# Optimization experiments

Measured on AMD Instinct MI355X. Metric: run time of the kernel, lower is better.

## Reference

```python
import jax, jax.numpy as jnp
import numpy as np

K = 1  # top-k experts per image


def cv_squared(v):
    # squared coefficient of variation; torch .var() is unbiased -> ddof=1
    eps = 1e-10
    m = v.mean()
    var = v.var(ddof=1)
    return jnp.where(jnp.abs(m) < eps, jnp.zeros((), v.dtype), var / (m * m + eps))


def setup_inputs() -> dict:
    key = jax.random.key(0)
    k0, k1, k2, k3 = jax.random.split(key, 4)
    B, H, W, C, E, HID = 64, 32, 32, 512, 5, 2048
    x = jax.random.normal(k0, (B, H, W, C), jnp.float32)
    # xavier-uniform-like scale for the gate
    gate_scale = float(np.sqrt(6.0 / (C + E)))
    w_gate = jax.random.uniform(k1, (C, E), jnp.float32, -gate_scale, gate_scale)
    W1 = jax.random.normal(k2, (E, C, HID), jnp.float32) * 0.02
    b1 = jnp.zeros((E, HID), jnp.float32)
    W2 = jax.random.normal(k3, (E, HID, C), jnp.float32) * 0.02
    b2 = jnp.zeros((E, C), jnp.float32)
    return {"x": x, "w_gate": w_gate, "W1": W1, "b1": b1, "W2": W2, "b2": b2}


def reference(x, w_gate, W1, b1, W2, b2):
    B, H, W_, C = x.shape
    E = w_gate.shape[1]
    xt = x.reshape(B, H * W_, C)              # [B, T, C] tokens
    xg = x.mean(axis=(1, 2))                  # [B, C] per-image gating feature

    # eval-mode noisy_top_k_gating (no noise): clean logits, clamp, top-k softmax
    logits = jnp.clip(xg @ w_gate, -50.0, 50.0)          # [B, E]
    top_logits, top_idx = jax.lax.top_k(logits, min(K + 1, E))
    tk_logits = top_logits[:, :K]
    tk_idx = top_idx[:, :K]                               # [B, K]
    tk_gates = jax.nn.softmax(tk_logits, axis=1)          # [B, K]
    gates = jnp.zeros_like(logits).at[jnp.arange(B)[:, None], tk_idx].set(tk_gates)

    importance = gates.sum(axis=0)                        # [E]
    load = (gates > 0).sum(axis=0).astype(jnp.float32)    # [E]
    loss = jnp.clip(cv_squared(importance) + cv_squared(load), 0.0, 1000.0)

    # dispatch: every token of image b goes through its top-K experts
    y = jnp.zeros_like(xt)
    for ki in range(K):
        idx = tk_idx[:, ki]                               # [B] expert id per image
        h = jnp.einsum('btd,bdh->bth', xt, W1[idx]) + b1[idx][:, None, :]
        h = jax.nn.gelu(h, approximate=False)             # torch nn.GELU default (erf)
        o = jnp.einsum('bth,bhd->btd', h, W2[idx]) + b2[idx][:, None, :]
        y = y + tk_gates[:, ki][:, None, None] * o

    return y.reshape(B, H, W_, C), loss
```

## Files before the change

### kernel.cpp

```cpp
#include <hip/hip_runtime.h>
#include <hip/hip_bf16.h>
#include <math.h>

typedef __attribute__((ext_vector_type(4))) float f4_t;
typedef __attribute__((ext_vector_type(8))) short s8_t;

constexpr int Bc = 64;
constexpr int Tc = 1024;
constexpr int Cc = 512;
constexpr int Ec = 5;
constexpr int HIDc = 2048;

__device__ __forceinline__ void async_copy16(const void* gsrc, void* ldst) {
  __builtin_amdgcn_global_load_lds(
      (const __attribute__((address_space(1))) unsigned int*)gsrc,
      (__attribute__((address_space(3))) unsigned int*)ldst, 16, 0, 0);
}


__global__ void k_partial(const float* __restrict__ x, float* __restrict__ part) {
  int b = blockIdx.x, p = blockIdx.y, tid = threadIdx.x;
  const float* xp = x + ((size_t)b * Tc + (size_t)p * 128) * Cc;
  float s0 = 0.f, s1 = 0.f;
  for (int t = 0; t < 128; ++t) {
    s0 += xp[(size_t)t * Cc + tid];
    s1 += xp[(size_t)t * Cc + tid + 256];
  }
  part[(size_t)(b * 8 + p) * Cc + tid] = s0;
  part[(size_t)(b * 8 + p) * Cc + tid + 256] = s1;
}

__global__ void k_xg_logits(const float* __restrict__ part, const float* __restrict__ wg,
                            float* __restrict__ logits) {
  __shared__ float xg[Cc];
  __shared__ float red[Ec][4];
  int b = blockIdx.x, tid = threadIdx.x;
  for (int c = tid; c < Cc; c += 256) {
    float s = 0.f;
#pragma unroll
    for (int p = 0; p < 8; ++p) s += part[(size_t)(b * 8 + p) * Cc + c];
    xg[c] = s * (1.0f / 1024.0f);
  }
  __syncthreads();
  float le[Ec] = {0.f, 0.f, 0.f, 0.f, 0.f};
  for (int c = tid; c < Cc; c += 256) {
    float v = xg[c];
#pragma unroll
    for (int e = 0; e < Ec; ++e) le[e] += v * wg[c * Ec + e];
  }
#pragma unroll
  for (int e = 0; e < Ec; ++e) {
    float v = le[e];
#pragma unroll
    for (int off = 32; off > 0; off >>= 1) v += __shfl_down(v, off);
    if ((tid & 63) == 0) red[e][tid >> 6] = v;
  }
  __syncthreads();
  if (tid < Ec) {
    float v = red[tid][0] + red[tid][1] + red[tid][2] + red[tid][3];
    v = fminf(fmaxf(v, -50.f), 50.f);
    logits[b * Ec + tid] = v;
  }
}

__global__ void k_gate(const float* __restrict__ logits, int* __restrict__ idx,
                       float* __restrict__ loss_out) {
  __shared__ int cnt[Ec];
  int tid = threadIdx.x;
  if (tid < Ec) cnt[tid] = 0;
  __syncthreads();
  if (tid < Bc) {
    const float* lb = logits + tid * Ec;
    int best = 0;
    float bv = lb[0];
#pragma unroll
    for (int e = 1; e < Ec; ++e) {
      float v = lb[e];
      if (v > bv) { bv = v; best = e; }
    }
    idx[tid] = best;
    atomicAdd(&cnt[best], 1);
  }
  __syncthreads();
  if (tid == 0) {
    const float mean = (float)Bc / (float)Ec;
    float var = 0.f;
#pragma unroll
    for (int e = 0; e < Ec; ++e) {
      float d = (float)cnt[e] - mean;
      var += d * d;
    }
    var *= (1.0f / (Ec - 1));
    float loss = 2.f * (var / (mean * mean + 1e-10f));
    loss = fminf(fmaxf(loss, 0.f), 1000.f);
    *loss_out = loss;
  }
}

__global__ void k_transpose_cvt(const float* __restrict__ src, __hip_bfloat16* __restrict__ dst,
                                int K, int N) {
  __shared__ float tile[32][33];
  int e = blockIdx.z;
  int kb = blockIdx.y * 32, nb = blockIdx.x * 32;
  const float* s = src + (size_t)e * K * N;
  __hip_bfloat16* d = dst + (size_t)e * K * N;
  int lx = threadIdx.x & 31, ly = threadIdx.x >> 5;
#pragma unroll
  for (int r = 0; r < 4; ++r) {
    int k = kb + ly + r * 8;
    tile[ly + r * 8][lx] = s[(size_t)k * N + nb + lx];
  }
  __syncthreads();
#pragma unroll
  for (int r = 0; r < 4; ++r) {
    int n = nb + ly + r * 8;
    d[(size_t)n * K + kb + lx] = __float2bfloat16(tile[lx][ly + r * 8]);
  }
}

__global__ void k_cvt_x(const float* __restrict__ src, ushort* __restrict__ dst, int n4) {
  int i = blockIdx.x * blockDim.x + threadIdx.x;
  int stride = gridDim.x * blockDim.x;
  const float4* s4 = (const float4*)src;
  ushort4* d4 = (ushort4*)dst;
  for (; i < n4; i += stride) {
    float4 v = s4[i];
    union { __hip_bfloat16 h[4]; ushort4 u; } cv;
    cv.h[0] = __float2bfloat16(v.x);
    cv.h[1] = __float2bfloat16(v.y);
    cv.h[2] = __float2bfloat16(v.z);
    cv.h[3] = __float2bfloat16(v.w);
    d4[i] = cv.u;
  }
}


__global__ __launch_bounds__(512, 2) void k_gemm1(
    const __hip_bfloat16* __restrict__ xbf, const __hip_bfloat16* __restrict__ w1t,
    const float* __restrict__ b1, const int* __restrict__ idx, int b0,
    __hip_bfloat16* __restrict__ h) {
  constexpr int K = Cc;
  constexpr int N = HIDc;
  constexpr int NT = K / 64;
  __shared__ short lds[2][2][256 * 64];

  int bz = blockIdx.z;
  int e = idx[b0 + bz];
  int m0 = blockIdx.y * 256;
  int n0 = blockIdx.x * 256;
  const short* Abase = (const short*)xbf + ((size_t)bz * Tc + m0) * K;
  const short* Bbase = (const short*)w1t + ((size_t)e * N + n0) * K;
  int tid = threadIdx.x;
  int l = tid & 63, w = tid >> 6;
  int wr = w >> 2, wc = w & 3;

  int s_row = tid >> 3;
  int s_col = (tid & 7) * 8;
  const short* gA[4];
  const short* gB[4];
#pragma unroll
  for (int i = 0; i < 4; ++i) {
    gA[i] = Abase + (size_t)(i * 64 + s_row) * K + s_col;
    gB[i] = Bbase + (size_t)(i * 64 + s_row) * K + s_col;
  }

  int a_off = (wr * 128 + (l & 15)) * 64 + (l >> 4) * 8;
  int b_off = (wc * 64 + (l & 15)) * 64 + (l >> 4) * 8;

  f4_t acc[8][4] = {};

#pragma unroll
  for (int i = 0; i < 4; ++i) {
    async_copy16(gA[i], (char*)&lds[0][0][0] + tid * 16 + i * 8192);
    async_copy16(gB[i], (char*)&lds[0][1][0] + tid * 16 + i * 8192);
  }
  __syncthreads();

  for (int t = 0; t < NT; ++t) {
    int cur = t & 1;
    const short* As = &lds[cur][0][0];
    const short* Bs = &lds[cur][1][0];
    if (t + 1 < NT) {
      int k0 = (t + 1) * 64;
#pragma unroll
      for (int i = 0; i < 4; ++i) {
        async_copy16(gA[i] + k0, (char*)&lds[cur ^ 1][0][0] + tid * 16 + i * 8192);
        async_copy16(gB[i] + k0, (char*)&lds[cur ^ 1][1][0] + tid * 16 + i * 8192);
      }
    }
#pragma unroll
    for (int kk = 0; kk < 2; ++kk) {
      s8_t a[8], b[4];
#pragma unroll
      for (int f = 0; f < 8; ++f)
        a[f] = *(const s8_t*)(As + a_off + f * 16 * 64 + kk * 32);
#pragma unroll
      for (int f = 0; f < 4; ++f)
        b[f] = *(const s8_t*)(Bs + b_off + f * 16 * 64 + kk * 32);
#pragma unroll
      for (int fm = 0; fm < 8; ++fm)
#pragma unroll
        for (int fn = 0; fn < 4; ++fn)
          acc[fm][fn] = __builtin_amdgcn_mfma_f32_16x16x32_bf16(a[fm], b[fn], acc[fm][fn], 0, 0, 0);
    }
    if (t + 1 < NT) __syncthreads();
  }

  __syncthreads();
  __hip_bfloat16* chunk = (__hip_bfloat16*)&lds[0][0][0] + w * 8192;
  const float* bias = b1 + (size_t)e * N;
#pragma unroll
  for (int fn = 0; fn < 4; ++fn) {
    int col = n0 + wc * 64 + fn * 16 + (l & 15);
    float bv = bias[col];
#pragma unroll
    for (int fm = 0; fm < 8; ++fm) {
      int row = fm * 16 + ((l >> 4) << 2);
#pragma unroll
      for (int j = 0; j < 4; ++j) {
        float v = acc[fm][fn][j] + bv;
        v = 0.5f * v * (1.0f + erff(v * 0.70710678118654752f));
        chunk[(row + j) * 64 + fn * 16 + (l & 15)] = __float2bfloat16(v);
      }
    }
  }
  short* hb = (short*)(h + (size_t)bz * Tc * N);
  int colb = n0 + wc * 64 + (l & 7) * 8;
#pragma unroll
  for (int p = 0; p < 16; ++p) {
    int row = p * 8 + (l >> 3);
    s8_t vrow = *(const s8_t*)((const short*)chunk + row * 64 + (l & 7) * 8);
    *(s8_t*)(hb + (size_t)(m0 + wr * 128 + row) * N + colb) = vrow;
  }
}

__global__ __launch_bounds__(512, 2) void k_gemm2(
    const __hip_bfloat16* __restrict__ h, const __hip_bfloat16* __restrict__ w2t,
    const float* __restrict__ b2, const int* __restrict__ idx, int b0,
    float* __restrict__ out) {
  constexpr int K = HIDc;
  constexpr int N = Cc;
  constexpr int NT = K / 64;
  __shared__ short lds[2][2][256 * 64];

  int bz = blockIdx.z;
  int e = idx[b0 + bz];
  int m0 = blockIdx.y * 256;
  int n0 = blockIdx.x * 256;
  const short* Abase = (const short*)h + ((size_t)bz * Tc + m0) * K;
  const short* Bbase = (const short*)w2t + ((size_t)e * N + n0) * K;
  int tid = threadIdx.x;
  int l = tid & 63, w = tid >> 6;
  int wr = w >> 2, wc = w & 3;

  int s_row = tid >> 3;
  int s_col = (tid & 7) * 8;
  const short* gA[4];
  const short* gB[4];
#pragma unroll
  for (int i = 0; i < 4; ++i) {
    gA[i] = Abase + (size_t)(i * 64 + s_row) * K + s_col;
    gB[i] = Bbase + (size_t)(i * 64 + s_row) * K + s_col;
  }

  int a_off = (wr * 128 + (l & 15)) * 64 + (l >> 4) * 8;
  int b_off = (wc * 64 + (l & 15)) * 64 + (l >> 4) * 8;

  f4_t acc[8][4] = {};

#pragma unroll
  for (int i = 0; i < 4; ++i) {
    async_copy16(gA[i], (char*)&lds[0][0][0] + tid * 16 + i * 8192);
    async_copy16(gB[i], (char*)&lds[0][1][0] + tid * 16 + i * 8192);
  }
  __syncthreads();

  for (int t = 0; t < NT; ++t) {
    int cur = t & 1;
    const short* As = &lds[cur][0][0];
    const short* Bs = &lds[cur][1][0];
    if (t + 1 < NT) {
      int k0 = (t + 1) * 64;
#pragma unroll
      for (int i = 0; i < 4; ++i) {
        async_copy16(gA[i] + k0, (char*)&lds[cur ^ 1][0][0] + tid * 16 + i * 8192);
        async_copy16(gB[i] + k0, (char*)&lds[cur ^ 1][1][0] + tid * 16 + i * 8192);
      }
    }
#pragma unroll
    for (int kk = 0; kk < 2; ++kk) {
      s8_t a[8], b[4];
#pragma unroll
      for (int f = 0; f < 8; ++f)
        a[f] = *(const s8_t*)(As + a_off + f * 16 * 64 + kk * 32);
#pragma unroll
      for (int f = 0; f < 4; ++f)
        b[f] = *(const s8_t*)(Bs + b_off + f * 16 * 64 + kk * 32);
#pragma unroll
      for (int fm = 0; fm < 8; ++fm)
#pragma unroll
        for (int fn = 0; fn < 4; ++fn)
          acc[fm][fn] = __builtin_amdgcn_mfma_f32_16x16x32_bf16(a[fm], b[fn], acc[fm][fn], 0, 0, 0);
    }
    if (t + 1 < NT) __syncthreads();
  }

  float* ob = out + (size_t)(b0 + bz) * Tc * N;
  const float* bias = b2 + (size_t)e * N;
#pragma unroll
  for (int fn = 0; fn < 4; ++fn) {
    int col = n0 + wc * 64 + fn * 16 + (l & 15);
    float bv = bias[col];
#pragma unroll
    for (int fm = 0; fm < 8; ++fm) {
      int rbase = m0 + wr * 128 + fm * 16 + ((l >> 4) << 2);
#pragma unroll
      for (int j = 0; j < 4; ++j) {
        ob[(size_t)(rbase + j) * N + col] = acc[fm][fn][j] + bv;
      }
    }
  }
}

extern "C" void kernel_launch(void* const* d_in, const int* in_sizes, int n_in,
                              void* d_out, int out_size, void* d_ws, size_t ws_size,
                              hipStream_t stream) {
  const float* x  = (const float*)d_in[0];
  const float* wg = (const float*)d_in[1];
  const float* W1 = (const float*)d_in[2];
  const float* b1 = (const float*)d_in[3];
  const float* W2 = (const float*)d_in[4];
  const float* b2 = (const float*)d_in[5];
  float* out = (float*)d_out;

  char* ws = (char*)d_ws;
  size_t off = 0;
  float* part = (float*)(ws + off); off += (size_t)Bc * 8 * Cc * 4;
  float* logits = (float*)(ws + off); off += (size_t)Bc * Ec * 4;
  int* idx = (int*)(ws + off); off += (size_t)Bc * 4;
  off = (off + 255) & ~(size_t)255;
  __hip_bfloat16* w1t = (__hip_bfloat16*)(ws + off); off += (size_t)Ec * HIDc * Cc * 2;
  __hip_bfloat16* w2t = (__hip_bfloat16*)(ws + off); off += (size_t)Ec * HIDc * Cc * 2;
  size_t dynoff = (off + 255) & ~(size_t)255;

  const size_t x_per_b = (size_t)Tc * Cc * 2;
  const size_t h_per_b = (size_t)Tc * HIDc * 2;
  size_t avail = ws_size > dynoff ? ws_size - dynoff : 0;
  int cb = (int)(avail / (x_per_b + h_per_b));
  if (cb > Bc) cb = Bc;
  if (cb < 1) cb = 1;

  k_partial<<<dim3(Bc, 8), 256, 0, stream>>>(x, part);
  k_xg_logits<<<dim3(Bc), 256, 0, stream>>>(part, wg, logits);
  k_gate<<<dim3(1), 256, 0, stream>>>(logits, idx, out + ((size_t)out_size - 1));

  k_transpose_cvt<<<dim3(HIDc / 32, Cc / 32, Ec), 256, 0, stream>>>(W1, w1t, Cc, HIDc);
  k_transpose_cvt<<<dim3(Cc / 32, HIDc / 32, Ec), 256, 0, stream>>>(W2, w2t, HIDc, Cc);

  __hip_bfloat16* xbf = (__hip_bfloat16*)(ws + dynoff);
  __hip_bfloat16* hbf = (__hip_bfloat16*)(ws + dynoff + (size_t)cb * x_per_b);

  for (int b0 = 0; b0 < Bc; b0 += cb) {
    int c = (Bc - b0) < cb ? (Bc - b0) : cb;
    int n4 = c * (Tc * Cc / 4);
    k_cvt_x<<<dim3(1024), 256, 0, stream>>>(x + (size_t)b0 * Tc * Cc, (ushort*)xbf, n4);
    k_gemm1<<<dim3(HIDc / 256, Tc / 256, c), 512, 0, stream>>>(xbf, w1t, b1, idx, b0, hbf);
    k_gemm2<<<dim3(Cc / 256, Tc / 256, c), 512, 0, stream>>>(hbf, w2t, b2, idx, b0, out);
  }
}
```

Before: 527.3 us.

## Fuse x mean and bf16 conversion, swizzle LDS, retile gemm1, cheaper GELU

After: 495.1 us. -6.1%, faster.

```diff
diff --git a/kernel.cpp b/kernel.cpp
--- a/kernel.cpp
+++ b/kernel.cpp
@@ -17,6 +17,47 @@
       (__attribute__((address_space(3))) unsigned int*)ldst, 16, 0, 0);
 }
 
+__device__ __forceinline__ float gelu_f(float v) {
+  float u = v * 0.70710678118654752f;
+  float ax = fabsf(u);
+  float t = __frcp_rn(1.0f + 0.3275911f * ax);
+  float p = t * (0.254829592f +
+           t * (-0.284496736f +
+           t * (1.421413741f +
+           t * (-1.453152027f +
+           t * 1.061405429f))));
+  float er = 1.0f - p * __expf(-u * u);
+  er = copysignf(er, u);
+  return 0.5f * v * (1.0f + er);
+}
+
+
+__global__ void k_prep(const float* __restrict__ x, ushort* __restrict__ xbf,
+                       float* __restrict__ part) {
+  int b = blockIdx.x, p = blockIdx.y, tid = threadIdx.x;
+  const float4* xp = (const float4*)(x + ((size_t)b * Tc + (size_t)p * 128) * Cc);
+  ushort4* op = (ushort4*)(xbf + ((size_t)b * Tc + (size_t)p * 128) * Cc);
+  int c4 = tid & 127, r0 = tid >> 7;
+  float4 s = {0.f, 0.f, 0.f, 0.f};
+  for (int r = r0; r < 128; r += 2) {
+    float4 v = xp[(size_t)r * 128 + c4];
+    s.x += v.x; s.y += v.y; s.z += v.z; s.w += v.w;
+    union { __hip_bfloat16 h[4]; ushort4 u; } cv;
+    cv.h[0] = __float2bfloat16(v.x);
+    cv.h[1] = __float2bfloat16(v.y);
+    cv.h[2] = __float2bfloat16(v.z);
+    cv.h[3] = __float2bfloat16(v.w);
+    op[(size_t)r * 128 + c4] = cv.u;
+  }
+  __shared__ float4 sh[128];
+  if (r0) sh[c4] = s;
+  __syncthreads();
+  if (!r0) {
+    float4 o = sh[c4];
+    s.x += o.x; s.y += o.y; s.z += o.z; s.w += o.w;
+    ((float4*)part)[(size_t)(b * 8 + p) * 128 + c4] = s;
+  }
+}
 
 __global__ void k_partial(const float* __restrict__ x, float* __restrict__ part) {
   int b = blockIdx.x, p = blockIdx.y, tid = threadIdx.x;
@@ -28,94 +69,6 @@
   }
   part[(size_t)(b * 8 + p) * Cc + tid] = s0;
   part[(size_t)(b * 8 + p) * Cc + tid + 256] = s1;
-}
-
-__global__ void k_xg_logits(const float* __restrict__ part, const float* __restrict__ wg,
-                            float* __restrict__ logits) {
-  __shared__ float xg[Cc];
-  __shared__ float red[Ec][4];
-  int b = blockIdx.x, tid = threadIdx.x;
-  for (int c = tid; c < Cc; c += 256) {
-    float s = 0.f;
-#pragma unroll
-    for (int p = 0; p < 8; ++p) s += part[(size_t)(b * 8 + p) * Cc + c];
-    xg[c] = s * (1.0f / 1024.0f);
-  }
-  __syncthreads();
-  float le[Ec] = {0.f, 0.f, 0.f, 0.f, 0.f};
-  for (int c = tid; c < Cc; c += 256) {
-    float v = xg[c];
-#pragma unroll
-    for (int e = 0; e < Ec; ++e) le[e] += v * wg[c * Ec + e];
-  }
-#pragma unroll
-  for (int e = 0; e < Ec; ++e) {
-    float v = le[e];
-#pragma unroll
-    for (int off = 32; off > 0; off >>= 1) v += __shfl_down(v, off);
-    if ((tid & 63) == 0) red[e][tid >> 6] = v;
-  }
-  __syncthreads();
-  if (tid < Ec) {
-    float v = red[tid][0] + red[tid][1] + red[tid][2] + red[tid][3];
-    v = fminf(fmaxf(v, -50.f), 50.f);
-    logits[b * Ec + tid] = v;
-  }
-}
-
-__global__ void k_gate(const float* __restrict__ logits, int* __restrict__ idx,
-                       float* __restrict__ loss_out) {
-  __shared__ int cnt[Ec];
-  int tid = threadIdx.x;
-  if (tid < Ec) cnt[tid] = 0;
-  __syncthreads();
-  if (tid < Bc) {
-    const float* lb = logits + tid * Ec;
-    int best = 0;
-    float bv = lb[0];
-#pragma unroll
-    for (int e = 1; e < Ec; ++e) {
-      float v = lb[e];
-      if (v > bv) { bv = v; best = e; }
-    }
-    idx[tid] = best;
-    atomicAdd(&cnt[best], 1);
-  }
-  __syncthreads();
-  if (tid == 0) {
-    const float mean = (float)Bc / (float)Ec;
-    float var = 0.f;
-#pragma unroll
-    for (int e = 0; e < Ec; ++e) {
-      float d = (float)cnt[e] - mean;
-      var += d * d;
-    }
-    var *= (1.0f / (Ec - 1));
-    float loss = 2.f * (var / (mean * mean + 1e-10f));
-    loss = fminf(fmaxf(loss, 0.f), 1000.f);
-    *loss_out = loss;
-  }
-}
-
-__global__ void k_transpose_cvt(const float* __restrict__ src, __hip_bfloat16* __restrict__ dst,
-                                int K, int N) {
-  __shared__ float tile[32][33];
-  int e = blockIdx.z;
-  int kb = blockIdx.y * 32, nb = blockIdx.x * 32;
-  const float* s = src + (size_t)e * K * N;
-  __hip_bfloat16* d = dst + (size_t)e * K * N;
-  int lx = threadIdx.x & 31, ly = threadIdx.x >> 5;
-#pragma unroll
-  for (int r = 0; r < 4; ++r) {
-    int k = kb + ly + r * 8;
-    tile[ly + r * 8][lx] = s[(size_t)k * N + nb + lx];
-  }
-  __syncthreads();
-#pragma unroll
-  for (int r = 0; r < 4; ++r) {
-    int n = nb + ly + r * 8;
-    d[(size_t)n * K + kb + lx] = __float2bfloat16(tile[lx][ly + r * 8]);
-  }
 }
 
 __global__ void k_cvt_x(const float* __restrict__ src, ushort* __restrict__ dst, int n4) {
@@ -134,175 +87,275 @@
   }
 }
 
-
-__global__ __launch_bounds__(512, 2) void k_gemm1(
+__global__ void k_xg_logits(const float* __restrict__ part, const float* __restrict__ wg,
+                            float* __restrict__ logits) {
+  __shared__ float xg[Cc];
+  __shared__ float red[Ec][4];
+  int b = blockIdx.x, tid = threadIdx.x;
+  for (int c = tid; c < Cc; c += 256) {
+    float s = 0.f;
+#pragma unroll
+    for (int p = 0; p < 8; ++p) s += part[(size_t)(b * 8 + p) * Cc + c];
+    xg[c] = s * (1.0f / 1024.0f);
+  }
+  __syncthreads();
+  float le[Ec] = {0.f, 0.f, 0.f, 0.f, 0.f};
+  for (int c = tid; c < Cc; c += 256) {
+    float v = xg[c];
+#pragma unroll
+    for (int e = 0; e < Ec; ++e) le[e] += v * wg[c * Ec + e];
+  }
+#pragma unroll
+  for (int e = 0; e < Ec; ++e) {
+    float v = le[e];
+#pragma unroll
+    for (int off = 32; off > 0; off >>= 1) v += __shfl_down(v, off);
+    if ((tid & 63) == 0) red[e][tid >> 6] = v;
+  }
+  __syncthreads();
+  if (tid < Ec) {
+    float v = red[tid][0] + red[tid][1] + red[tid][2] + red[tid][3];
+    v = fminf(fmaxf(v, -50.f), 50.f);
+    logits[b * Ec + tid] = v;
+  }
+}
+
+__global__ void k_gate(const float* __restrict__ logits, int* __restrict__ idx,
+                       float* __restrict__ loss_out) {
+  __shared__ int cnt[Ec];
+  int tid = threadIdx.x;
+  if (tid < Ec) cnt[tid] = 0;
+  __syncthreads();
+  if (tid < Bc) {
+    const float* lb = logits + tid * Ec;
+    int best = 0;
+    float bv = lb[0];
+#pragma unroll
+    for (int e = 1; e < Ec; ++e) {
+      float v = lb[e];
+      if (v > bv) { bv = v; best = e; }
+    }
+    idx[tid] = best;
+    atomicAdd(&cnt[best], 1);
+  }
+  __syncthreads();
+  if (tid == 0) {
+    const float mean = (float)Bc / (float)Ec;
+    float var = 0.f;
+#pragma unroll
+    for (int e = 0; e < Ec; ++e) {
+      float d = (float)cnt[e] - mean;
+      var += d * d;
+    }
+    var *= (1.0f / (Ec - 1));
+    float loss = 2.f * (var / (mean * mean + 1e-10f));
+    loss = fminf(fmaxf(loss, 0.f), 1000.f);
+    *loss_out = loss;
+  }
+}
+
+__global__ void k_transpose_cvt(const float* __restrict__ src, __hip_bfloat16* __restrict__ dst,
+                                int K, int N) {
+  __shared__ float tile[32][33];
+  int e = blockIdx.z;
+  int kb = blockIdx.y * 32, nb = blockIdx.x * 32;
+  const float* s = src + (size_t)e * K * N;
+  __hip_bfloat16* d = dst + (size_t)e * K * N;
+  int lx = threadIdx.x & 31, ly = threadIdx.x >> 5;
+#pragma unroll
+  for (int r = 0; r < 4; ++r) {
+    int k = kb + ly + r * 8;
+    tile[ly + r * 8][lx] = s[(size_t)k * N + nb + lx];
+  }
+  __syncthreads();
+#pragma unroll
+  for (int r = 0; r < 4; ++r) {
+    int n = nb + ly + r * 8;
+    d[(size_t)n * K + kb + lx] = __float2bfloat16(tile[lx][ly + r * 8]);
+  }
+}
+
+
+__global__ __launch_bounds__(256, 2) void k_gemm1(
     const __hip_bfloat16* __restrict__ xbf, const __hip_bfloat16* __restrict__ w1t,
-    const float* __restrict__ b1, const int* __restrict__ idx, int b0,
+    const float* __restrict__ b1, const int* __restrict__ idx, int b0, int nz,
     __hip_bfloat16* __restrict__ h) {
   constexpr int K = Cc;
   constexpr int N = HIDc;
   constexpr int NT = K / 64;
-  __shared__ short lds[2][2][256 * 64];
-
-  int bz = blockIdx.z;
+  constexpr int NBX = N / 128, NBY = Tc / 128;
+  __shared__ short lds[2][2][128 * 64];
+
+  int nwg = NBX * NBY * nz;
+  int cpx = nwg >> 3;
+  int lg = (blockIdx.x & 7) * cpx + (blockIdx.x >> 3);
+  int bx = lg % NBX, by = (lg / NBX) % NBY, bz = lg / (NBX * NBY);
+
   int e = idx[b0 + bz];
-  int m0 = blockIdx.y * 256;
-  int n0 = blockIdx.x * 256;
-  const short* Abase = (const short*)xbf + ((size_t)bz * Tc + m0) * K;
-  const short* Bbase = (const short*)w1t + ((size_t)e * N + n0) * K;
-  int tid = threadIdx.x;
-  int l = tid & 63, w = tid >> 6;
-  int wr = w >> 2, wc = w & 3;
-
-  int s_row = tid >> 3;
-  int s_col = (tid & 7) * 8;
+  int m0 = by * 128, n0 = bx * 128;
+  const short* Ab = (const short*)xbf + ((size_t)bz * Tc + m0) * K;
+  const short* Bb = (const short*)w1t + ((size_t)e * N + n0) * K;
+  int tid = threadIdx.x, l = tid & 63, w = tid >> 6;
+  int wr = w >> 1, wc = w & 1;
+
   const short* gA[4];
   const short* gB[4];
+  int loff[4];
 #pragma unroll
   for (int i = 0; i < 4; ++i) {
-    gA[i] = Abase + (size_t)(i * 64 + s_row) * K + s_col;
-    gB[i] = Bbase + (size_t)(i * 64 + s_row) * K + s_col;
-  }
-
-  int a_off = (wr * 128 + (l & 15)) * 64 + (l >> 4) * 8;
-  int b_off = (wc * 64 + (l & 15)) * 64 + (l >> 4) * 8;
-
-  f4_t acc[8][4] = {};
+    int sp = i * 256 + tid;
+    int r = sp >> 3;
+    int c8 = ((sp & 7) ^ (r & 7)) << 3;
+    gA[i] = Ab + (size_t)r * K + c8;
+    gB[i] = Bb + (size_t)r * K + c8;
+    loff[i] = sp * 16;
+  }
+
+  int arow = wr * 64 + (l & 15);
+  int brow = wc * 64 + (l & 15);
+  int s0 = (((l >> 4)) ^ (l & 7)) << 4;
+  int s1 = (((l >> 4) + 4) ^ (l & 7)) << 4;
+
+  f4_t acc[4][4] = {};
 
 #pragma unroll
   for (int i = 0; i < 4; ++i) {
-    async_copy16(gA[i], (char*)&lds[0][0][0] + tid * 16 + i * 8192);
-    async_copy16(gB[i], (char*)&lds[0][1][0] + tid * 16 + i * 8192);
+    async_copy16(gA[i], (char*)&lds[0][0][0] + loff[i]);
+    async_copy16(gB[i], (char*)&lds[0][1][0] + loff[i]);
   }
   __syncthreads();
 
   for (int t = 0; t < NT; ++t) {
     int cur = t & 1;
-    const short* As = &lds[cur][0][0];
-    const short* Bs = &lds[cur][1][0];
     if (t + 1 < NT) {
       int k0 = (t + 1) * 64;
 #pragma unroll
       for (int i = 0; i < 4; ++i) {
-        async_copy16(gA[i] + k0, (char*)&lds[cur ^ 1][0][0] + tid * 16 + i * 8192);
-        async_copy16(gB[i] + k0, (char*)&lds[cur ^ 1][1][0] + tid * 16 + i * 8192);
+        async_copy16(gA[i] + k0, (char*)&lds[cur ^ 1][0][0] + loff[i]);
+        async_copy16(gB[i] + k0, (char*)&lds[cur ^ 1][1][0] + loff[i]);
       }
     }
+    const char* As = (const char*)&lds[cur][0][0];
+    const char* Bs = (const char*)&lds[cur][1][0];
 #pragma unroll
     for (int kk = 0; kk < 2; ++kk) {
-      s8_t a[8], b[4];
-#pragma unroll
-      for (int f = 0; f < 8; ++f)
-        a[f] = *(const s8_t*)(As + a_off + f * 16 * 64 + kk * 32);
-#pragma unroll
-      for (int f = 0; f < 4; ++f)
-        b[f] = *(const s8_t*)(Bs + b_off + f * 16 * 64 + kk * 32);
-#pragma unroll
-      for (int fm = 0; fm < 8; ++fm)
+      int sk = kk ? s1 : s0;
+      s8_t a[4], b[4];
+#pragma unroll
+      for (int f = 0; f < 4; ++f) a[f] = *(const s8_t*)(As + (arow + f * 16) * 128 + sk);
+#pragma unroll
+      for (int f = 0; f < 4; ++f) b[f] = *(const s8_t*)(Bs + (brow + f * 16) * 128 + sk);
+#pragma unroll
+      for (int fm = 0; fm < 4; ++fm)
 #pragma unroll
         for (int fn = 0; fn < 4; ++fn)
           acc[fm][fn] = __builtin_amdgcn_mfma_f32_16x16x32_bf16(a[fm], b[fn], acc[fm][fn], 0, 0, 0);
     }
-    if (t + 1 < NT) __syncthreads();
-  }
-
-  __syncthreads();
-  __hip_bfloat16* chunk = (__hip_bfloat16*)&lds[0][0][0] + w * 8192;
+    __syncthreads();
+  }
+
+  short* chunk = &lds[0][0][0] + w * (64 * 80);
   const float* bias = b1 + (size_t)e * N;
 #pragma unroll
   for (int fn = 0; fn < 4; ++fn) {
-    int col = n0 + wc * 64 + fn * 16 + (l & 15);
-    float bv = bias[col];
-#pragma unroll
-    for (int fm = 0; fm < 8; ++fm) {
-      int row = fm * 16 + ((l >> 4) << 2);
+    float bv = bias[n0 + wc * 64 + fn * 16 + (l & 15)];
+#pragma unroll
+    for (int fm = 0; fm < 4; ++fm) {
+      int r4 = fm * 16 + ((l >> 4) << 2);
 #pragma unroll
       for (int j = 0; j < 4; ++j) {
-        float v = acc[fm][fn][j] + bv;
-        v = 0.5f * v * (1.0f + erff(v * 0.70710678118654752f));
-        chunk[(row + j) * 64 + fn * 16 + (l & 15)] = __float2bfloat16(v);
+        float v = gelu_f(acc[fm][fn][j] + bv);
+        chunk[(r4 + j) * 80 + fn * 16 + (l & 15)] =
+            (short)__bfloat16_as_ushort(__float2bfloat16(v));
       }
     }
   }
   short* hb = (short*)(h + (size_t)bz * Tc * N);
-  int colb = n0 + wc * 64 + (l & 7) * 8;
-#pragma unroll
-  for (int p = 0; p < 16; ++p) {
-    int row = p * 8 + (l >> 3);
-    s8_t vrow = *(const s8_t*)((const short*)chunk + row * 64 + (l & 7) * 8);
-    *(s8_t*)(hb + (size_t)(m0 + wr * 128 + row) * N + colb) = vrow;
+  int cc = (l & 7) * 8;
+#pragma unroll
+  for (int p = 0; p < 8; ++p) {
+    int rr = p * 8 + (l >> 3);
+    s8_t v = *(const s8_t*)(chunk + rr * 80 + cc);
+    *(s8_t*)(hb + (size_t)(m0 + wr * 64 + rr) * N + n0 + wc * 64 + cc) = v;
   }
 }
 
 __global__ __launch_bounds__(512, 2) void k_gemm2(
     const __hip_bfloat16* __restrict__ h, const __hip_bfloat16* __restrict__ w2t,
-    const float* __restrict__ b2, const int* __restrict__ idx, int b0,
+    const float* __restrict__ b2, const int* __restrict__ idx, int b0, int nz,
     float* __restrict__ out) {
   constexpr int K = HIDc;
   constexpr int N = Cc;
   constexpr int NT = K / 64;
+  constexpr int NBX = N / 256, NBY = Tc / 256;
   __shared__ short lds[2][2][256 * 64];
 
-  int bz = blockIdx.z;
+  int nwg = NBX * NBY * nz;
+  int cpx = nwg >> 3;
+  int lg = (blockIdx.x & 7) * cpx + (blockIdx.x >> 3);
+  int bx = lg % NBX, by = (lg / NBX) % NBY, bz = lg / (NBX * NBY);
+
   int e = idx[b0 + bz];
-  int m0 = blockIdx.y * 256;
-  int n0 = blockIdx.x * 256;
-  const short* Abase = (const short*)h + ((size_t)bz * Tc + m0) * K;
-  const short* Bbase = (const short*)w2t + ((size_t)e * N + n0) * K;
-  int tid = threadIdx.x;
-  int l = tid & 63, w = tid >> 6;
+  int m0 = by * 256, n0 = bx * 256;
+  const short* Ab = (const short*)h + ((size_t)bz * Tc + m0) * K;
+  const short* Bb = (const short*)w2t + ((size_t)e * N + n0) * K;
+  int tid = threadIdx.x, l = tid & 63, w = tid >> 6;
   int wr = w >> 2, wc = w & 3;
 
-  int s_row = tid >> 3;
-  int s_col = (tid & 7) * 8;
   const short* gA[4];
   const short* gB[4];
+  int loff[4];
 #pragma unroll
   for (int i = 0; i < 4; ++i) {
-    gA[i] = Abase + (size_t)(i * 64 + s_row) * K + s_col;
-    gB[i] = Bbase + (size_t)(i * 64 + s_row) * K + s_col;
-  }
-
-  int a_off = (wr * 128 + (l & 15)) * 64 + (l >> 4) * 8;
-  int b_off = (wc * 64 + (l & 15)) * 64 + (l >> 4) * 8;
+    int sp = i * 512 + tid;
+    int r = sp >> 3;
+    int c8 = ((sp & 7) ^ (r & 7)) << 3;
+    gA[i] = Ab + (size_t)r * K + c8;
+    gB[i] = Bb + (size_t)r * K + c8;
+    loff[i] = sp * 16;
+  }
+
+  int arow = wr * 128 + (l & 15);
+  int brow = wc * 64 + (l & 15);
+  int s0 = (((l >> 4)) ^ (l & 7)) << 4;
+  int s1 = (((l >> 4) + 4) ^ (l & 7)) << 4;
 
   f4_t acc[8][4] = {};
 
 #pragma unroll
   for (int i = 0; i < 4; ++i) {
-    async_copy16(gA[i], (char*)&lds[0][0][0] + tid * 16 + i * 8192);
-    async_copy16(gB[i], (char*)&lds[0][1][0] + tid * 16 + i * 8192);
+    async_copy16(gA[i], (char*)&lds[0][0][0] + loff[i]);
+    async_copy16(gB[i], (char*)&lds[0][1][0] + loff[i]);
   }
   __syncthreads();
 
   for (int t = 0; t < NT; ++t) {
     int cur = t & 1;
-    const short* As = &lds[cur][0][0];
-    const short* Bs = &lds[cur][1][0];
     if (t + 1 < NT) {
       int k0 = (t + 1) * 64;
 #pragma unroll
       for (int i = 0; i < 4; ++i) {
-        async_copy16(gA[i] + k0, (char*)&lds[cur ^ 1][0][0] + tid * 16 + i * 8192);
-        async_copy16(gB[i] + k0, (char*)&lds[cur ^ 1][1][0] + tid * 16 + i * 8192);
+        async_copy16(gA[i] + k0, (char*)&lds[cur ^ 1][0][0] + loff[i]);
+        async_copy16(gB[i] + k0, (char*)&lds[cur ^ 1][1][0] + loff[i]);
       }
     }
+    const char* As = (const char*)&lds[cur][0][0];
+    const char* Bs = (const char*)&lds[cur][1][0];
 #pragma unroll
     for (int kk = 0; kk < 2; ++kk) {
+      int sk = kk ? s1 : s0;
       s8_t a[8], b[4];
 #pragma unroll
-      for (int f = 0; f < 8; ++f)
-        a[f] = *(const s8_t*)(As + a_off + f * 16 * 64 + kk * 32);
-#pragma unroll
-      for (int f = 0; f < 4; ++f)
-        b[f] = *(const s8_t*)(Bs + b_off + f * 16 * 64 + kk * 32);
+      for (int f = 0; f < 8; ++f) a[f] = *(const s8_t*)(As + (arow + f * 16) * 128 + sk);
+#pragma unroll
+      for (int f = 0; f < 4; ++f) b[f] = *(const s8_t*)(Bs + (brow + f * 16) * 128 + sk);
 #pragma unroll
       for (int fm = 0; fm < 8; ++fm)
 #pragma unroll
         for (int fn = 0; fn < 4; ++fn)
           acc[fm][fn] = __builtin_amdgcn_mfma_f32_16x16x32_bf16(a[fm], b[fn], acc[fm][fn], 0, 0, 0);
     }
-    if (t + 1 < NT) __syncthreads();
+    __syncthreads();
   }
 
   float* ob = out + (size_t)(b0 + bz) * Tc * N;
@@ -343,28 +396,51 @@
   __hip_bfloat16* w2t = (__hip_bfloat16*)(ws + off); off += (size_t)Ec * HIDc * Cc * 2;
   size_t dynoff = (off + 255) & ~(size_t)255;
 
+  const size_t x_all = (size_t)Bc * Tc * Cc * 2;
   const size_t x_per_b = (size_t)Tc * Cc * 2;
   const size_t h_per_b = (size_t)Tc * HIDc * 2;
-  size_t avail = ws_size > dynoff ? ws_size - dynoff : 0;
-  int cb = (int)(avail / (x_per_b + h_per_b));
-  if (cb > Bc) cb = Bc;
-  if (cb < 1) cb = 1;
-
-  k_partial<<<dim3(Bc, 8), 256, 0, stream>>>(x, part);
-  k_xg_logits<<<dim3(Bc), 256, 0, stream>>>(part, wg, logits);
-  k_gate<<<dim3(1), 256, 0, stream>>>(logits, idx, out + ((size_t)out_size - 1));
 
   k_transpose_cvt<<<dim3(HIDc / 32, Cc / 32, Ec), 256, 0, stream>>>(W1, w1t, Cc, HIDc);
   k_transpose_cvt<<<dim3(Cc / 32, HIDc / 32, Ec), 256, 0, stream>>>(W2, w2t, HIDc, Cc);
 
-  __hip_bfloat16* xbf = (__hip_bfloat16*)(ws + dynoff);
-  __hip_bfloat16* hbf = (__hip_bfloat16*)(ws + dynoff + (size_t)cb * x_per_b);
-
-  for (int b0 = 0; b0 < Bc; b0 += cb) {
-    int c = (Bc - b0) < cb ? (Bc - b0) : cb;
-    int n4 = c * (Tc * Cc / 4);
-    k_cvt_x<<<dim3(1024), 256, 0, stream>>>(x + (size_t)b0 * Tc * Cc, (ushort*)xbf, n4);
-    k_gemm1<<<dim3(HIDc / 256, Tc / 256, c), 512, 0, stream>>>(xbf, w1t, b1, idx, b0, hbf);
-    k_gemm2<<<dim3(Cc / 256, Tc / 256, c), 512, 0, stream>>>(hbf, w2t, b2, idx, b0, out);
-  }
-}
+  if (ws_size >= dynoff + x_all + h_per_b) {
+    __hip_bfloat16* xbf = (__hip_bfloat16*)(ws + dynoff);
+    __hip_bfloat16* hbf = (__hip_bfloat16*)(ws + dynoff + x_all);
+    int cb = (int)((ws_size - dynoff - x_all) / h_per_b);
+    if (cb > Bc) cb = Bc;
+
+    k_prep<<<dim3(Bc, 8), 256, 0, stream>>>(x, (ushort*)xbf, part);
+    k_xg_logits<<<dim3(Bc), 256, 0, stream>>>(part, wg, logits);
+    k_gate<<<dim3(1), 256, 0, stream>>>(logits, idx, out + ((size_t)out_size - 1));
+
+    for (int b0 = 0; b0 < Bc; b0 += cb) {
+      int c = (Bc - b0) < cb ? (Bc - b0) : cb;
+      const __hip_bfloat16* xc = xbf + (size_t)b0 * Tc * Cc;
+      k_gemm1<<<dim3((HIDc / 128) * (Tc / 128) * c), 256, 0, stream>>>(
+          xc, w1t, b1, idx, b0, c, hbf);
+      k_gemm2<<<dim3((Cc / 256) * (Tc / 256) * c), 512, 0, stream>>>(
+          hbf, w2t, b2, idx, b0, c, out);
+    }
+  } else {
+    size_t avail = ws_size > dynoff ? ws_size - dynoff : 0;
+    int cb = (int)(avail / (x_per_b + h_per_b));
+    if (cb > Bc) cb = Bc;
+    if (cb < 1) cb = 1;
+    __hip_bfloat16* xbf = (__hip_bfloat16*)(ws + dynoff);
+    __hip_bfloat16* hbf = (__hip_bfloat16*)(ws + dynoff + (size_t)cb * x_per_b);
+
+    k_partial<<<dim3(Bc, 8), 256, 0, stream>>>(x, part);
+    k_xg_logits<<<dim3(Bc), 256, 0, stream>>>(part, wg, logits);
+    k_gate<<<dim3(1), 256, 0, stream>>>(logits, idx, out + ((size_t)out_size - 1));
+
+    for (int b0 = 0; b0 < Bc; b0 += cb) {
+      int c = (Bc - b0) < cb ? (Bc - b0) : cb;
+      int n4 = c * (Tc * Cc / 4);
+      k_cvt_x<<<dim3(1024), 256, 0, stream>>>(x + (size_t)b0 * Tc * Cc, (ushort*)xbf, n4);
+      k_gemm1<<<dim3((HIDc / 128) * (Tc / 128) * c), 256, 0, stream>>>(
+          xbf, w1t, b1, idx, 0 + b0, c, hbf);
+      k_gemm2<<<dim3((Cc / 256) * (Tc / 256) * c), 512, 0, stream>>>(
+          hbf, w2t, b2, idx, b0, c, out);
+    }
+  }
+}
```
